# Kernel tuning notes

Hardware: AMD Instinct MI355X
Metric: run time of the kernel (lower is better)

The kernel has to match this reference:

```python
import jax, jax.numpy as jnp
import numpy as np

HEADS = 16
DIM_HEAD = 64
QUERY_DIM = 1024
INNER = HEADS * DIM_HEAD


def setup_inputs() -> dict:
    key = jax.random.key(0)
    ks = jax.random.split(key, 6)
    b, n = 4, 2048
    s = 0.02
    return {
        "x": jax.random.normal(ks[0], (b, n, QUERY_DIM), dtype=jnp.float32),
        "Wq": jax.random.normal(ks[1], (QUERY_DIM, INNER), dtype=jnp.float32) * s,
        "Wk": jax.random.normal(ks[2], (QUERY_DIM, INNER), dtype=jnp.float32) * s,
        "Wv": jax.random.normal(ks[3], (QUERY_DIM, INNER), dtype=jnp.float32) * s,
        "Wo": jax.random.normal(ks[4], (INNER, QUERY_DIM), dtype=jnp.float32) * s,
        "bo": jax.random.normal(ks[5], (QUERY_DIM,), dtype=jnp.float32) * s,
    }


def reference(x, Wq, Wk, Wv, Wo, bo):
    b, n, _ = x.shape
    scale = DIM_HEAD ** (-0.5)
    # project and split heads: [b, n, inner] -> [b, h, n, d]
    def split(t):
        return t.reshape(b, n, HEADS, DIM_HEAD).transpose(0, 2, 1, 3)
    q = split(x @ Wq)
    k = split(x @ Wk)
    v = split(x @ Wv)
    sim = jnp.einsum('bhid,bhjd->bhij', q, k) * scale  # [b, h, n, n]
    attn = jax.nn.softmax(sim, axis=-1)
    out = jnp.einsum('bhij,bhjd->bhid', attn, v)  # [b, h, n, d]
    out = out.transpose(0, 2, 1, 3).reshape(b, n, INNER)
    return out @ Wo + bo
```

## Files before the change

### kernel.cpp

```cpp
#include <hip/hip_runtime.h>

typedef __attribute__((ext_vector_type(8))) short bf16x8;
typedef __attribute__((ext_vector_type(4))) float f32x4;
typedef __attribute__((ext_vector_type(16))) float f32x16;
typedef __attribute__((ext_vector_type(2))) unsigned u32x2;

__device__ __forceinline__ unsigned short f2b(float f) {
  union { float f; unsigned u; } x; x.f = f;
  unsigned r = x.u + 0x7fffu + ((x.u >> 16) & 1u);
  return (unsigned short)(r >> 16);
}

__device__ __forceinline__ int cvt_pk_bf16(float lo, float hi) {
  int r;
  asm("v_cvt_pk_bf16_f32 %0, %1, %2" : "=v"(r) : "v"(lo), "v"(hi));
  return r;
}

__device__ __forceinline__ float exp2_fast(float x) {
#if __has_builtin(__builtin_amdgcn_exp2f)
  return __builtin_amdgcn_exp2f(x);
#else
  return __expf(x * 0.69314718055994531f);
#endif
}

__device__ __forceinline__ void gl_lds16(const unsigned short* g, unsigned short* l) {
  __builtin_amdgcn_global_load_lds(
      (const __attribute__((address_space(1))) unsigned int*)(unsigned long long)g,
      (__attribute__((address_space(3))) unsigned int*)(unsigned)(unsigned long long)l,
      16, 0, 0);
}

#define MFMA(a, b, c) __builtin_amdgcn_mfma_f32_16x16x32_bf16((a), (b), (c), 0, 0, 0)
#define MFMA32(a, b, c) __builtin_amdgcn_mfma_f32_32x32x16_bf16((a), (b), (c), 0, 0, 0)

__global__ __launch_bounds__(256) void convert_x(const float* __restrict__ x,
                                                 unsigned short* __restrict__ xb) {
  int i = (blockIdx.x * 256 + threadIdx.x) * 4;
  float4 v = *(const float4*)(x + i);
  ushort4 o;
  o.x = f2b(v.x); o.y = f2b(v.y); o.z = f2b(v.z); o.w = f2b(v.w);
  *(ushort4*)(xb + i) = o;
}

__global__ __launch_bounds__(256) void transpose_w(const float* __restrict__ wq, const float* __restrict__ wk,
                                                   const float* __restrict__ wv, const float* __restrict__ wo,
                                                   unsigned short* __restrict__ tq, unsigned short* __restrict__ tk,
                                                   unsigned short* __restrict__ tv, unsigned short* __restrict__ to_) {
  int z = blockIdx.z;
  const float* W = (z == 0) ? wq : (z == 1) ? wk : (z == 2) ? wv : wo;
  unsigned short* T = (z == 0) ? tq : (z == 1) ? tk : (z == 2) ? tv : to_;
  float scale = (z == 0) ? 0.125f * 1.4426950408889634f : 1.0f;
  __shared__ float tile[64][65];
  int tr = blockIdx.y * 64, tc = blockIdx.x * 64;
  int t = threadIdx.x;
  int col = t & 63, r0 = (t >> 6) * 16;
#pragma unroll
  for (int r = 0; r < 16; r++)
    tile[r0 + r][col] = W[(long)(tr + r0 + r) * 1024 + tc + col];
  __syncthreads();
  int k = t & 63, n0 = (t >> 6) * 16;
#pragma unroll
  for (int n = 0; n < 16; n++)
    T[(long)(tc + n0 + n) * 1024 + tr + k] = f2b(tile[k][n0 + n] * scale);
}

__device__ __forceinline__ void gemm_core_256(const unsigned short* __restrict__ A,
                                              const unsigned short* __restrict__ BT,
                                              int m0, int n0,
                                              unsigned short* As, unsigned short* Bs,
                                              f32x4 acc[8][4]) {
  const int t = threadIdx.x;
  const int lane = t & 63;
  const int wid = t >> 6;
  const int wr = wid >> 2, wc = wid & 3;
  const int c = lane & 15, g = lane >> 4;

#define STAGE_HALF(MAT, base, kt_, dst, hh)                                           \
  {                                                                                   \
    _Pragma("unroll")                                                                 \
    for (int j = 0; j < 2; j++) {                                                     \
      int idx = j * 512 + t;                                                          \
      int srow = idx >> 3, pc = idx & 7;                                              \
      int sc = pc ^ (srow & 7);                                                       \
      gl_lds16(MAT + (long)((base) + (hh) * 128 + srow) * 1024 + (kt_) * 64 + sc * 8, \
               (dst) + (hh) * 8192 + idx * 8);                                        \
    }                                                                                 \
  }

  STAGE_HALF(A, m0, 0, As, 0);
  STAGE_HALF(A, m0, 0, As, 1);
  STAGE_HALF(BT, n0, 0, Bs, 0);
  STAGE_HALF(BT, n0, 0, Bs, 1);

  for (int kt = 0; kt < 16; kt++) {
    unsigned short* Ab = As + (kt & 1) * 16384;
    unsigned short* Bb = Bs + (kt & 1) * 16384;
    unsigned short* An = As + ((kt & 1) ^ 1) * 16384;
    unsigned short* Bn = Bs + ((kt & 1) ^ 1) * 16384;
    asm volatile("s_waitcnt vmcnt(0)" ::: "memory");
    __builtin_amdgcn_s_barrier();

    bf16x8 bfr[2][4];
#pragma unroll
    for (int ph = 0; ph < 4; ph++) {
      const int qm = ph & 1, ks = ph >> 1;
      bf16x8 af[4];
      if (qm == 0) {
#pragma unroll
        for (int ni = 0; ni < 4; ni++) {
          int row = wc * 64 + ni * 16 + c;
          bfr[ks][ni] = *(const bf16x8*)(Bb + row * 64 + ((ks * 4 + g) ^ (row & 7)) * 8);
        }
      }
#pragma unroll
      for (int i = 0; i < 4; i++) {
        int row = wr * 128 + (qm * 4 + i) * 16 + c;
        af[i] = *(const bf16x8*)(Ab + row * 64 + ((ks * 4 + g) ^ (row & 7)) * 8);
      }
      if (kt + 1 < 16) {
        if (ph == 0) STAGE_HALF(A, m0, kt + 1, An, 0)
        else if (ph == 1) STAGE_HALF(A, m0, kt + 1, An, 1)
        else if (ph == 2) STAGE_HALF(BT, n0, kt + 1, Bn, 0)
        else STAGE_HALF(BT, n0, kt + 1, Bn, 1)
      }
      __builtin_amdgcn_s_barrier();
      __builtin_amdgcn_s_setprio(1);
#pragma unroll
      for (int i = 0; i < 4; i++)
#pragma unroll
        for (int ni = 0; ni < 4; ni++)
          acc[qm * 4 + i][ni] = MFMA(af[i], bfr[ks][ni], acc[qm * 4 + i][ni]);
      __builtin_amdgcn_s_setprio(0);
      __builtin_amdgcn_s_barrier();
    }
  }
#undef STAGE_HALF
}

__global__ __launch_bounds__(512) void gemm_qkv(const unsigned short* __restrict__ xb,
                                                const unsigned short* __restrict__ wtq,
                                                const unsigned short* __restrict__ wtk,
                                                const unsigned short* __restrict__ wtv,
                                                unsigned short* __restrict__ Qw,
                                                unsigned short* __restrict__ Kw,
                                                unsigned short* __restrict__ Vtw) {
  __shared__ unsigned short As[2 * 16384], Bs[2 * 16384];
  int m0 = blockIdx.x * 256;
  int nglob0 = blockIdx.y * 256;
  int which = nglob0 >> 10;
  const unsigned short* BT = (which == 0) ? wtq : (which == 1) ? wtk : wtv;
  int n0 = nglob0 & 1023;
  f32x4 acc[8][4] = {};
  gemm_core_256(xb, BT, m0, n0, As, Bs, acc);

  const int t = threadIdx.x;
  const int lane = t & 63, wid = t >> 6;
  const int wr = wid >> 2, wc = wid & 3;
  const int c = lane & 15, g = lane >> 4;
  int b = m0 >> 11;
  int ibase = m0 & 2047;
#pragma unroll
  for (int mi = 0; mi < 8; mi++) {
    int irow0 = ibase + wr * 128 + mi * 16 + g * 4;
#pragma unroll
    for (int ni = 0; ni < 4; ni++) {
      int nl = n0 + wc * 64 + ni * 16 + c;
      int h = nl >> 6, d = nl & 63;
      if (which == 2) {
        ushort4 pk;
        pk.x = f2b(acc[mi][ni][0]); pk.y = f2b(acc[mi][ni][1]);
        pk.z = f2b(acc[mi][ni][2]); pk.w = f2b(acc[mi][ni][3]);
        *(ushort4*)(Vtw + ((long)(b * 16 + h) * 64 + d) * 2048 + irow0) = pk;
      } else {
        unsigned short* dst = (which == 0) ? Qw : Kw;
#pragma unroll
        for (int r = 0; r < 4; r++)
          dst[((long)(b * 16 + h) * 2048 + irow0 + r) * 64 + d] = f2b(acc[mi][ni][r]);
      }
    }
  }
}

__global__ __launch_bounds__(512) void gemm_out(const unsigned short* __restrict__ Ao,
                                                const unsigned short* __restrict__ wto,
                                                const float* __restrict__ bias,
                                                float* __restrict__ out) {
  __shared__ unsigned short As[2 * 16384], Bs[2 * 16384];
  int m0 = blockIdx.x * 256;
  int n0 = blockIdx.y * 256;
  f32x4 acc[8][4] = {};
  gemm_core_256(Ao, wto, m0, n0, As, Bs, acc);

  const int t = threadIdx.x;
  const int lane = t & 63, wid = t >> 6;
  const int wr = wid >> 2, wc = wid & 3;
  const int c = lane & 15, g = lane >> 4;
#pragma unroll
  for (int mi = 0; mi < 8; mi++)
#pragma unroll
    for (int ni = 0; ni < 4; ni++) {
      int col = n0 + wc * 64 + ni * 16 + c;
      float bv = bias[col];
#pragma unroll
      for (int r = 0; r < 4; r++) {
        int row = m0 + wr * 128 + mi * 16 + g * 4 + r;
        out[(long)row * 1024 + col] = acc[mi][ni][r] + bv;
      }
    }
}

__global__ __launch_bounds__(512) void attn(const unsigned short* __restrict__ Qw,
                                            const unsigned short* __restrict__ Kw,
                                            const unsigned short* __restrict__ Vtw,
                                            unsigned short* __restrict__ Ow) {
  int ib = blockIdx.y * 8 + blockIdx.x;
  int xcd = ib & 7, j = ib >> 3;
  int bh = xcd * 8 + (j >> 3);
  int qt = j & 7;
  int t = threadIdx.x;
  int lane = t & 63, wid = t >> 6;
  int c5 = lane & 31, h = lane >> 5;
  __shared__ unsigned short Ks[2][64 * 64];
  __shared__ unsigned short Vs[2][64 * 64];

  const unsigned short* Qp = Qw + ((long)bh * 2048 + qt * 256 + wid * 32 + c5) * 64 + h * 8;
  bf16x8 qf[4];
#pragma unroll
  for (int dK = 0; dK < 4; dK++) qf[dK] = *(const bf16x8*)(Qp + dK * 16);

  f32x16 oacc0 = {}, oacc1 = {};
  float ls0 = 0.f, ls1 = 0.f, ls2 = 0.f, ls3 = 0.f;

  const unsigned short* Kbase = Kw + (long)bh * 2048 * 64;
  const unsigned short* Vbase = Vtw + (long)bh * 64 * 2048;

#define STAGE(jt_, buf_)                                                              \
  {                                                                                   \
    int row = t >> 3, ch = t & 7;                                                     \
    int sw = ch ^ (row & 7);                                                          \
    gl_lds16(Kbase + (long)((jt_) * 64 + row) * 64 + sw * 8, &Ks[buf_][t * 8]);       \
    gl_lds16(Vbase + (long)row * 2048 + (jt_) * 64 + sw * 8, &Vs[buf_][t * 8]);       \
  }

  STAGE(0, 0);

  union FR { int i[4]; bf16x8 v; };

  for (int jt = 0; jt < 32; jt++) {
    int buf = jt & 1;
    __syncthreads();
    if (jt + 1 < 32) STAGE(jt + 1, buf ^ 1);

    f32x16 s0 = {}, s1 = {};
#pragma unroll
    for (int dK = 0; dK < 4; dK++) {
      int sw = ((dK * 2 + h) ^ (c5 & 7)) * 8;
      bf16x8 k0 = *(const bf16x8*)(&Ks[buf][c5 * 64 + sw]);
      bf16x8 k1 = *(const bf16x8*)(&Ks[buf][c5 * 64 + sw + 2048]);
      s0 = MFMA32(k0, qf[dK], s0);
      s1 = MFMA32(k1, qf[dK], s1);
    }

    int pk[2][4][2];
#pragma unroll
    for (int q2 = 0; q2 < 4; q2++) {
      float a0 = exp2_fast(s0[q2 * 4 + 0]), a1 = exp2_fast(s0[q2 * 4 + 1]);
      float a2 = exp2_fast(s0[q2 * 4 + 2]), a3 = exp2_fast(s0[q2 * 4 + 3]);
      ls0 += a0 + a1; ls1 += a2 + a3;
      pk[0][q2][0] = cvt_pk_bf16(a0, a1);
      pk[0][q2][1] = cvt_pk_bf16(a2, a3);
      float b0 = exp2_fast(s1[q2 * 4 + 0]), b1 = exp2_fast(s1[q2 * 4 + 1]);
      float b2 = exp2_fast(s1[q2 * 4 + 2]), b3 = exp2_fast(s1[q2 * 4 + 3]);
      ls2 += b0 + b1; ls3 += b2 + b3;
      pk[1][q2][0] = cvt_pk_bf16(b0, b1);
      pk[1][q2][1] = cvt_pk_bf16(b2, b3);
    }

#pragma unroll
    for (int kblk = 0; kblk < 4; kblk++) {
      int kvb = kblk >> 1, e2c = (kblk & 1) * 2;
      u32x2 p0 = __builtin_amdgcn_permlane32_swap((unsigned)pk[kvb][e2c][0],
                                                  (unsigned)pk[kvb][e2c + 1][0], false, false);
      u32x2 p1 = __builtin_amdgcn_permlane32_swap((unsigned)pk[kvb][e2c][1],
                                                  (unsigned)pk[kvb][e2c + 1][1], false, false);
      FR fr;
      fr.i[0] = (int)p0[0];
      fr.i[1] = (int)p1[0];
      fr.i[2] = (int)p0[1];
      fr.i[3] = (int)p1[1];
      int sw = ((kblk * 2 + h) ^ (c5 & 7)) * 8;
      bf16x8 v0 = *(const bf16x8*)(&Vs[buf][c5 * 64 + sw]);
      bf16x8 v1 = *(const bf16x8*)(&Vs[buf][c5 * 64 + sw + 2048]);
      oacc0 = MFMA32(v0, fr.v, oacc0);
      oacc1 = MFMA32(v1, fr.v, oacc1);
    }
  }
#undef STAGE

  float lsum = ls0 + ls1 + ls2 + ls3;
  lsum += __shfl_xor(lsum, 32);
  float inv = 1.0f / lsum;
  int b = bh >> 4, hh = bh & 15;
  long row = (long)b * 2048 + qt * 256 + wid * 32 + c5;
  unsigned short* orow = Ow + row * 1024 + hh * 64;
#pragma unroll
  for (int dblk = 0; dblk < 2; dblk++) {
#pragma unroll
    for (int q2 = 0; q2 < 4; q2++) {
      float o0 = (dblk ? oacc1 : oacc0)[q2 * 4 + 0] * inv;
      float o1 = (dblk ? oacc1 : oacc0)[q2 * 4 + 1] * inv;
      float o2 = (dblk ? oacc1 : oacc0)[q2 * 4 + 2] * inv;
      float o3 = (dblk ? oacc1 : oacc0)[q2 * 4 + 3] * inv;
      ushort4 pkv;
      pkv.x = f2b(o0); pkv.y = f2b(o1); pkv.z = f2b(o2); pkv.w = f2b(o3);
      *(ushort4*)(orow + dblk * 32 + q2 * 8 + h * 4) = pkv;
    }
  }
}

extern "C" void kernel_launch(void* const* d_in, const int* in_sizes, int n_in,
                              void* d_out, int out_size, void* d_ws, size_t ws_size,
                              hipStream_t stream) {
  const float* x  = (const float*)d_in[0];
  const float* Wq = (const float*)d_in[1];
  const float* Wk = (const float*)d_in[2];
  const float* Wv = (const float*)d_in[3];
  const float* Wo = (const float*)d_in[4];
  const float* bo = (const float*)d_in[5];
  float* out = (float*)d_out;

  char* ws = (char*)d_ws;
  unsigned short* xb  = (unsigned short*)(ws);
  unsigned short* wtq = (unsigned short*)(ws + 16777216);
  unsigned short* wtk = (unsigned short*)(ws + 16777216 + 2097152);
  unsigned short* wtv = (unsigned short*)(ws + 16777216 + 2 * 2097152);
  unsigned short* wto = (unsigned short*)(ws + 16777216 + 3 * 2097152);
  unsigned short* Qw  = (unsigned short*)(ws + 25165824);
  unsigned short* Kw  = (unsigned short*)(ws + 25165824 + 16777216);
  unsigned short* Vtw = (unsigned short*)(ws + 25165824 + 2 * 16777216);
  unsigned short* Aow = xb;

  convert_x<<<8192, 256, 0, stream>>>(x, xb);
  transpose_w<<<dim3(16, 16, 4), 256, 0, stream>>>(Wq, Wk, Wv, Wo, wtq, wtk, wtv, wto);
  gemm_qkv<<<dim3(32, 12), 512, 0, stream>>>(xb, wtq, wtk, wtv, Qw, Kw, Vtw);
  attn<<<dim3(8, 64), 512, 0, stream>>>(Qw, Kw, Vtw, Aow);
  gemm_out<<<dim3(32, 4), 512, 0, stream>>>(Aow, wto, bo, out);
}
```

Measured before the change: 184.5 us.

## Shrink GEMM tiles to 256x128 and restructure staging into half-K pipelined phases

Changes the QKV and output projection GEMMs from 256x256 to 256x128 tiles, which doubles the grid (384→768 and 128→256 blocks) so more of the GPU's compute units are filled. The K tile is split into two 32-wide halves with a new swizzle, and partial vmcnt waits allow the next tile's loads to overlap with MFMA work. Shared memory use per block also drops. The cost is lower arithmetic intensity per block, since each block reloads A for fewer output columns.

```diff
diff --git a/kernel.cpp b/kernel.cpp
--- a/kernel.cpp
+++ b/kernel.cpp
@@ -66,77 +66,96 @@
     T[(long)(tc + n0 + n) * 1024 + tr + k] = f2b(tile[k][n0 + n] * scale);
 }
 
-__device__ __forceinline__ void gemm_core_256(const unsigned short* __restrict__ A,
-                                              const unsigned short* __restrict__ BT,
-                                              int m0, int n0,
-                                              unsigned short* As, unsigned short* Bs,
-                                              f32x4 acc[8][4]) {
+__device__ __forceinline__ void gemm_core_256x128(const unsigned short* __restrict__ A,
+                                                  const unsigned short* __restrict__ BT,
+                                                  int m0, int n0,
+                                                  unsigned short* As, unsigned short* Bs,
+                                                  f32x4 acc[8][2]) {
   const int t = threadIdx.x;
   const int lane = t & 63;
   const int wid = t >> 6;
   const int wr = wid >> 2, wc = wid & 3;
   const int c = lane & 15, g = lane >> 4;
 
-#define STAGE_HALF(MAT, base, kt_, dst, hh)                                           \
-  {                                                                                   \
-    _Pragma("unroll")                                                                 \
-    for (int j = 0; j < 2; j++) {                                                     \
-      int idx = j * 512 + t;                                                          \
-      int srow = idx >> 3, pc = idx & 7;                                              \
-      int sc = pc ^ (srow & 7);                                                       \
-      gl_lds16(MAT + (long)((base) + (hh) * 128 + srow) * 1024 + (kt_) * 64 + sc * 8, \
-               (dst) + (hh) * 8192 + idx * 8);                                        \
-    }                                                                                 \
-  }
-
-  STAGE_HALF(A, m0, 0, As, 0);
-  STAGE_HALF(A, m0, 0, As, 1);
-  STAGE_HALF(BT, n0, 0, Bs, 0);
-  STAGE_HALF(BT, n0, 0, Bs, 1);
+#define SA(hk, kt_, db)                                                                \
+  {                                                                                    \
+    _Pragma("unroll")                                                                  \
+    for (int j = 0; j < 2; j++) {                                                      \
+      int idx = j * 512 + t;                                                           \
+      int row = idx >> 2, pl = idx & 3;                                                \
+      int sc = (hk) * 4 + (pl ^ ((row >> 1) & 3));                                     \
+      gl_lds16(A + (long)(m0 + row) * 1024 + (kt_) * 64 + sc * 8,                      \
+               As + (db) * 16384 + (hk) * 8192 + idx * 8);                             \
+    }                                                                                  \
+  }
+#define SB(hk, kt_, db)                                                                \
+  {                                                                                    \
+    int row = t >> 2, pl = t & 3;                                                      \
+    int sc = (hk) * 4 + (pl ^ ((row >> 1) & 3));                                       \
+    gl_lds16(BT + (long)(n0 + row) * 1024 + (kt_) * 64 + sc * 8,                       \
+             Bs + (db) * 8192 + (hk) * 4096 + t * 8);                                  \
+  }
+
+#define RD_B(dstv, ks, buf)                                                            \
+  {                                                                                    \
+    _Pragma("unroll")                                                                  \
+    for (int ni = 0; ni < 2; ni++) {                                                   \
+      int row = wc * 32 + ni * 16 + c;                                                 \
+      dstv[ni] = *(const bf16x8*)(Bs + (buf) * 8192 + (ks) * 4096 + row * 32 +         \
+                                  ((g ^ ((row >> 1) & 3)) * 8));                       \
+    }                                                                                  \
+  }
+#define RD_A(dstv, ks, qm, buf)                                                        \
+  {                                                                                    \
+    _Pragma("unroll")                                                                  \
+    for (int i = 0; i < 4; i++) {                                                      \
+      int row = wr * 128 + ((qm) * 4 + i) * 16 + c;                                    \
+      dstv[i] = *(const bf16x8*)(As + (buf) * 16384 + (ks) * 8192 + row * 32 +         \
+                                 ((g ^ ((row >> 1) & 3)) * 8));                        \
+    }                                                                                  \
+  }
+#define DO_MFMA(afv, bfv, qm)                                                          \
+  __builtin_amdgcn_s_setprio(1);                                                       \
+  _Pragma("unroll")                                                                    \
+  for (int i = 0; i < 4; i++)                                                          \
+    _Pragma("unroll")                                                                  \
+    for (int ni = 0; ni < 2; ni++)                                                     \
+      acc[(qm) * 4 + i][ni] = MFMA(afv[i], bfv[ni], acc[(qm) * 4 + i][ni]);            \
+  __builtin_amdgcn_s_setprio(0);
+
+#define SYNC(n)                                                                        \
+  asm volatile("s_waitcnt vmcnt(" #n ")" ::: "memory");                                \
+  __builtin_amdgcn_s_barrier();                                                        \
+  __builtin_amdgcn_sched_barrier(0);
+
+  SA(0, 0, 0); SB(0, 0, 0); SA(1, 0, 0); SB(1, 0, 0);
 
   for (int kt = 0; kt < 16; kt++) {
-    unsigned short* Ab = As + (kt & 1) * 16384;
-    unsigned short* Bb = Bs + (kt & 1) * 16384;
-    unsigned short* An = As + ((kt & 1) ^ 1) * 16384;
-    unsigned short* Bn = Bs + ((kt & 1) ^ 1) * 16384;
-    asm volatile("s_waitcnt vmcnt(0)" ::: "memory");
-    __builtin_amdgcn_s_barrier();
-
-    bf16x8 bfr[2][4];
-#pragma unroll
-    for (int ph = 0; ph < 4; ph++) {
-      const int qm = ph & 1, ks = ph >> 1;
-      bf16x8 af[4];
-      if (qm == 0) {
-#pragma unroll
-        for (int ni = 0; ni < 4; ni++) {
-          int row = wc * 64 + ni * 16 + c;
-          bfr[ks][ni] = *(const bf16x8*)(Bb + row * 64 + ((ks * 4 + g) ^ (row & 7)) * 8);
-        }
-      }
-#pragma unroll
-      for (int i = 0; i < 4; i++) {
-        int row = wr * 128 + (qm * 4 + i) * 16 + c;
-        af[i] = *(const bf16x8*)(Ab + row * 64 + ((ks * 4 + g) ^ (row & 7)) * 8);
-      }
-      if (kt + 1 < 16) {
-        if (ph == 0) STAGE_HALF(A, m0, kt + 1, An, 0)
-        else if (ph == 1) STAGE_HALF(A, m0, kt + 1, An, 1)
-        else if (ph == 2) STAGE_HALF(BT, n0, kt + 1, Bn, 0)
-        else STAGE_HALF(BT, n0, kt + 1, Bn, 1)
-      }
-      __builtin_amdgcn_s_barrier();
-      __builtin_amdgcn_s_setprio(1);
-#pragma unroll
-      for (int i = 0; i < 4; i++)
-#pragma unroll
-        for (int ni = 0; ni < 4; ni++)
-          acc[qm * 4 + i][ni] = MFMA(af[i], bfr[ks][ni], acc[qm * 4 + i][ni]);
-      __builtin_amdgcn_s_setprio(0);
-      __builtin_amdgcn_s_barrier();
-    }
-  }
-#undef STAGE_HALF
+    int buf = kt & 1, nb = buf ^ 1;
+    bf16x8 af[4], bf[2];
+    SYNC(3)
+    RD_B(bf, 0, buf);
+    RD_A(af, 0, 0, buf);
+    if (kt < 15) SA(0, kt + 1, nb);
+    DO_MFMA(af, bf, 0)
+    RD_A(af, 0, 1, buf);
+    if (kt < 15) SB(0, kt + 1, nb);
+    DO_MFMA(af, bf, 1)
+    if (kt < 15) { SYNC(3) } else { SYNC(0) }
+    RD_B(bf, 1, buf);
+    RD_A(af, 1, 0, buf);
+    if (kt < 15) SA(1, kt + 1, nb);
+    DO_MFMA(af, bf, 0)
+    RD_A(af, 1, 1, buf);
+    if (kt < 15) SB(1, kt + 1, nb);
+    DO_MFMA(af, bf, 1)
+  }
+#undef SA
+#undef SB
+#undef RD_A
+#undef RD_B
+#undef DO_MFMA
+#undef SYNC
 }
 
 __global__ __launch_bounds__(512) void gemm_qkv(const unsigned short* __restrict__ xb,
@@ -146,14 +165,14 @@
                                                 unsigned short* __restrict__ Qw,
                                                 unsigned short* __restrict__ Kw,
                                                 unsigned short* __restrict__ Vtw) {
-  __shared__ unsigned short As[2 * 16384], Bs[2 * 16384];
+  __shared__ unsigned short As[2 * 16384], Bs[2 * 8192];
   int m0 = blockIdx.x * 256;
-  int nglob0 = blockIdx.y * 256;
+  int nglob0 = blockIdx.y * 128;
   int which = nglob0 >> 10;
   const unsigned short* BT = (which == 0) ? wtq : (which == 1) ? wtk : wtv;
   int n0 = nglob0 & 1023;
-  f32x4 acc[8][4] = {};
-  gemm_core_256(xb, BT, m0, n0, As, Bs, acc);
+  f32x4 acc[8][2] = {};
+  gemm_core_256x128(xb, BT, m0, n0, As, Bs, acc);
 
   const int t = threadIdx.x;
   const int lane = t & 63, wid = t >> 6;
@@ -165,8 +184,8 @@
   for (int mi = 0; mi < 8; mi++) {
     int irow0 = ibase + wr * 128 + mi * 16 + g * 4;
 #pragma unroll
-    for (int ni = 0; ni < 4; ni++) {
-      int nl = n0 + wc * 64 + ni * 16 + c;
+    for (int ni = 0; ni < 2; ni++) {
+      int nl = n0 + wc * 32 + ni * 16 + c;
       int h = nl >> 6, d = nl & 63;
       if (which == 2) {
         ushort4 pk;
@@ -187,11 +206,11 @@
                                                 const unsigned short* __restrict__ wto,
                                                 const float* __restrict__ bias,
                                                 float* __restrict__ out) {
-  __shared__ unsigned short As[2 * 16384], Bs[2 * 16384];
+  __shared__ unsigned short As[2 * 16384], Bs[2 * 8192];
   int m0 = blockIdx.x * 256;
-  int n0 = blockIdx.y * 256;
-  f32x4 acc[8][4] = {};
-  gemm_core_256(Ao, wto, m0, n0, As, Bs, acc);
+  int n0 = blockIdx.y * 128;
+  f32x4 acc[8][2] = {};
+  gemm_core_256x128(Ao, wto, m0, n0, As, Bs, acc);
 
   const int t = threadIdx.x;
   const int lane = t & 63, wid = t >> 6;
@@ -200,8 +219,8 @@
 #pragma unroll
   for (int mi = 0; mi < 8; mi++)
 #pragma unroll
-    for (int ni = 0; ni < 4; ni++) {
-      int col = n0 + wc * 64 + ni * 16 + c;
+    for (int ni = 0; ni < 2; ni++) {
+      int col = n0 + wc * 32 + ni * 16 + c;
       float bv = bias[col];
 #pragma unroll
       for (int r = 0; r < 4; r++) {
@@ -344,7 +363,7 @@
 
   convert_x<<<8192, 256, 0, stream>>>(x, xb);
   transpose_w<<<dim3(16, 16, 4), 256, 0, stream>>>(Wq, Wk, Wv, Wo, wtq, wtk, wtv, wto);
-  gemm_qkv<<<dim3(32, 12), 512, 0, stream>>>(xb, wtq, wtk, wtv, Qw, Kw, Vtw);
+  gemm_qkv<<<dim3(32, 24), 512, 0, stream>>>(xb, wtq, wtk, wtv, Qw, Kw, Vtw);
   attn<<<dim3(8, 64), 512, 0, stream>>>(Qw, Kw, Vtw, Aow);
-  gemm_out<<<dim3(32, 4), 512, 0, stream>>>(Aow, wto, bo, out);
-}
+  gemm_out<<<dim3(32, 8), 512, 0, stream>>>(Aow, wto, bo, out);
+}
```

New measurement: 167.3 us. -9.4%, faster.
